# Optimization experiments

Measured on AMD Instinct MI355X. Metric: run time of the kernel, lower is better.

Reference implementation:

```python
import jax, jax.numpy as jnp
import numpy as np

N_NODES = 100000
N_EDGES = 800000
IN_DIM, HID_DIM, OUT_DIM = 128, 256, 128


def setup_inputs() -> dict:
    key = jax.random.key(0)
    k1, k2, k3, k4, k5 = jax.random.split(key, 5)
    x = jax.random.normal(k1, (N_NODES, IN_DIM), dtype=jnp.float32)
    edge_index = jax.random.randint(k2, (2, N_EDGES), 0, N_NODES, dtype=jnp.int64)
    edge_weight = jax.random.uniform(k3, (N_EDGES,), dtype=jnp.float32)
    W1 = jax.random.normal(k4, (IN_DIM, HID_DIM), dtype=jnp.float32) * 0.02
    b1 = jnp.zeros((HID_DIM,), dtype=jnp.float32)
    W2 = jax.random.normal(k5, (HID_DIM, OUT_DIM), dtype=jnp.float32) * 0.02
    b2 = jnp.zeros((OUT_DIM,), dtype=jnp.float32)
    return {"x": x, "edge_index": edge_index, "edge_weight": edge_weight,
            "W1": W1, "b1": b1, "W2": W2, "b2": b2}


def reference(x, edge_index, edge_weight, W1, b1, W2, b2):
    # GCNConv (normalize=True, add_self_loops=False), two layers with ReLU.
    # Dropout is identity at inference.
    row = edge_index[0]  # source nodes (E,)
    col = edge_index[1]  # target nodes (E,)
    n = x.shape[0]

    # Symmetric normalization: deg at target, norm = d^-1/2[row]*w*d^-1/2[col]
    deg = jax.ops.segment_sum(edge_weight, col, num_segments=n)  # (N,)
    dis = jnp.where(deg > 0, jax.lax.rsqrt(deg), 0.0)
    norm = dis[row] * edge_weight * dis[col]  # (E,)

    def gcn_conv(h, W, b):
        h = h @ W                                   # (N, F_out)
        msg = h[row] * norm[:, None]                # (E, F_out) gather+scale
        agg = jax.ops.segment_sum(msg, col, num_segments=n)  # scatter-add
        return agg + b

    h = jax.nn.relu(gcn_conv(x.astype(jnp.float32), W1, b1))
    return gcn_conv(h, W2, b2)
```

## Files before the change

### kernel.cpp

```cpp
#include <hip/hip_runtime.h>
#include <hip/hip_bf16.h>
#include <cstdint>
#include <cstddef>

#define N_NODES 100000
#define N_EDGES 800000
#define IN_DIM 128
#define HID_DIM 256
#define OUT_DIM 128

#define DEG_SCALE 2097152.0f
#define DEG_INV   (1.0f / 2097152.0f)

typedef __attribute__((ext_vector_type(8))) short bf16x8;
typedef __attribute__((ext_vector_type(4))) float f32x4;

__device__ __forceinline__ unsigned short f32_to_bf16(float f) {
    __hip_bfloat16 b = __float2bfloat16(f);
    return *reinterpret_cast<unsigned short*>(&b);
}
__device__ __forceinline__ float bf16_lo(uint32_t u) {
    uint32_t v = u << 16; return *reinterpret_cast<float*>(&v);
}
__device__ __forceinline__ float bf16_hi(uint32_t u) {
    uint32_t v = u & 0xffff0000u; return *reinterpret_cast<float*>(&v);
}

#define HIST_BLOCKS 3125
#define XB_BLOCKS 12500

__global__ void hist_prep_kernel(const int* __restrict__ ei,
                                 const float* __restrict__ ew,
                                 unsigned long long* __restrict__ cnt64,
                                 int* __restrict__ rank,
                                 const float* __restrict__ x,
                                 uint32_t* __restrict__ xb,
                                 const float* __restrict__ W1,
                                 unsigned short* __restrict__ W1F,
                                 const float* __restrict__ W2,
                                 unsigned short* __restrict__ W2F) {
    int b = blockIdx.x;
    if (b < HIST_BLOCKS) {
        int e = b * 256 + threadIdx.x;
        int c = ei[N_EDGES + e];
        uint32_t wfix = (uint32_t)(ew[e] * DEG_SCALE + 0.5f);
        unsigned long long add = (1ULL << 32) | (unsigned long long)wfix;
        unsigned long long old = atomicAdd(&cnt64[c], add);
        rank[e] = (int)(old >> 32);
        return;
    }
    b -= HIST_BLOCKS;
    if (b < XB_BLOCKS) {
        int i = b * 256 + threadIdx.x;
        float4 v = ((const float4*)x)[i];
        uint32_t lo = (uint32_t)f32_to_bf16(v.x) | ((uint32_t)f32_to_bf16(v.y) << 16);
        uint32_t hi = (uint32_t)f32_to_bf16(v.z) | ((uint32_t)f32_to_bf16(v.w) << 16);
        ((uint2*)xb)[i] = make_uint2(lo, hi);
    } else if (b < XB_BLOCKS + 128) {
        int idx = (b - XB_BLOCKS) * 256 + threadIdx.x;
        int j = idx & 7, lane = (idx >> 3) & 63;
        int nt = (idx >> 9) & 3, ks = (idx >> 11) & 3;
        int wc = (idx >> 13) & 1, nh = (idx >> 14) & 1;
        int fr = lane & 15, fq = lane >> 4;
        int row = nh * 128 + wc * 64 + nt * 16 + fr;
        int kk = ks * 32 + fq * 8 + j;
        W1F[idx] = f32_to_bf16(W1[kk * HID_DIM + row]);
    } else {
        int idx = (b - XB_BLOCKS - 128) * 256 + threadIdx.x;
        int j = idx & 7, lane = (idx >> 3) & 63;
        int nt = (idx >> 9) & 3, ks = (idx >> 11) & 3;
        int wc = (idx >> 13) & 1, nh = (idx >> 14) & 1;
        int fr = lane & 15, fq = lane >> 4;
        int n = wc * 64 + nt * 16 + fr;
        int kk = nh * 128 + ks * 32 + fq * 8 + j;
        W2F[idx] = f32_to_bf16(W2[kk * OUT_DIM + n]);
    }
}

__global__ void scan1_kernel(const unsigned long long* __restrict__ cnt64,
                             int* __restrict__ out, int* __restrict__ bsums,
                             float* __restrict__ dis, int n) {
    __shared__ int tmp[256];
    int t = threadIdx.x;
    int i = blockIdx.x * 256 + t;
    unsigned long long cv = (i < n) ? cnt64[i] : 0ULL;
    int v = (int)(cv >> 32);
    tmp[t] = v;
    __syncthreads();
    for (int off = 1; off < 256; off <<= 1) {
        int u = (t >= off) ? tmp[t - off] : 0;
        __syncthreads();
        tmp[t] += u;
        __syncthreads();
    }
    if (i < n) {
        out[i] = tmp[t] - v;
        uint32_t wf = (uint32_t)cv;
        dis[i] = wf ? rsqrtf((float)wf * DEG_INV) : 0.f;
    }
    if (t == 255) bsums[blockIdx.x] = tmp[255];
}

__global__ void scan23_kernel(int* __restrict__ rowp, const int* __restrict__ bsums,
                              int n, int total) {
    __shared__ int red[256];
    int b = blockIdx.x, t = threadIdx.x;
    int s = 0;
    for (int i = t; i < b; i += 256) s += bsums[i];
    red[t] = s;
    __syncthreads();
    for (int off = 128; off > 0; off >>= 1) {
        if (t < off) red[t] += red[t + off];
        __syncthreads();
    }
    int pre = red[0];
    int i = b * 256 + t;
    if (i == 0) rowp[n] = total;
    if (i < n) rowp[i] += pre;
}

__global__ void place_kernel(const int* __restrict__ ei,
                             const float* __restrict__ ew,
                             const int* __restrict__ rank,
                             const int* __restrict__ rowp,
                             const float* __restrict__ dis,
                             int2* __restrict__ pairs) {
    int e = blockIdx.x * 256 + threadIdx.x;
    if (e >= N_EDGES) return;
    int s = ei[e];
    int c = ei[N_EDGES + e];
    int pos = rowp[c] + rank[e];
    float wn = ew[e] * dis[s] * dis[c];
    pairs[pos] = make_int2(s, __float_as_int(wn));
}

__device__ __forceinline__ void acc_edge(float w, uint4 u, float* a) {
    a[0] += w * bf16_lo(u.x); a[1] += w * bf16_hi(u.x);
    a[2] += w * bf16_lo(u.y); a[3] += w * bf16_hi(u.y);
    a[4] += w * bf16_lo(u.z); a[5] += w * bf16_hi(u.z);
    a[6] += w * bf16_lo(u.w); a[7] += w * bf16_hi(u.w);
}

template <bool OUT_BF16>
__global__ void aggregate_kernel(const uint4* __restrict__ feat,
                                 const int* __restrict__ rowp,
                                 const int2* __restrict__ pairs,
                                 void* __restrict__ out_v,
                                 const float* __restrict__ bias) {
    int gtid = blockIdx.x * blockDim.x + threadIdx.x;
    int node = gtid >> 4;
    int lane = threadIdx.x & 15;
    if (node >= N_NODES) return;
    int beg = rowp[node], end = rowp[node + 1];
    float a[8] = {};

    int j = beg;
    for (; j + 8 <= end; j += 8) {
        int2 p[8]; uint4 u[8];
        #pragma unroll
        for (int q = 0; q < 8; ++q) p[q] = pairs[j + q];
        #pragma unroll
        for (int q = 0; q < 8; ++q) u[q] = feat[(size_t)p[q].x * 16 + lane];
        #pragma unroll
        for (int q = 0; q < 8; ++q) acc_edge(__int_as_float(p[q].y), u[q], a);
    }
    int r = end - j;
    if (r > 4) {
        int2 p[8]; uint4 u[8];
        #pragma unroll
        for (int q = 0; q < 8; ++q) {
            int idx = (j + q < end) ? j + q : beg;
            p[q] = pairs[idx];
        }
        #pragma unroll
        for (int q = 0; q < 8; ++q) u[q] = feat[(size_t)p[q].x * 16 + lane];
        #pragma unroll
        for (int q = 0; q < 8; ++q) {
            float w = (j + q < end) ? __int_as_float(p[q].y) : 0.f;
            acc_edge(w, u[q], a);
        }
    } else if (r > 0) {
        int2 p[4]; uint4 u[4];
        #pragma unroll
        for (int q = 0; q < 4; ++q) {
            int idx = (j + q < end) ? j + q : beg;
            p[q] = pairs[idx];
        }
        #pragma unroll
        for (int q = 0; q < 4; ++q) u[q] = feat[(size_t)p[q].x * 16 + lane];
        #pragma unroll
        for (int q = 0; q < 4; ++q) {
            float w = (j + q < end) ? __int_as_float(p[q].y) : 0.f;
            acc_edge(w, u[q], a);
        }
    }

    if (bias) {
        float4 b0 = ((const float4*)bias)[lane * 2];
        float4 b1 = ((const float4*)bias)[lane * 2 + 1];
        a[0] += b0.x; a[1] += b0.y; a[2] += b0.z; a[3] += b0.w;
        a[4] += b1.x; a[5] += b1.y; a[6] += b1.z; a[7] += b1.w;
    }
    if (OUT_BF16) {
        uint4 o;
        o.x = (uint32_t)f32_to_bf16(a[0]) | ((uint32_t)f32_to_bf16(a[1]) << 16);
        o.y = (uint32_t)f32_to_bf16(a[2]) | ((uint32_t)f32_to_bf16(a[3]) << 16);
        o.z = (uint32_t)f32_to_bf16(a[4]) | ((uint32_t)f32_to_bf16(a[5]) << 16);
        o.w = (uint32_t)f32_to_bf16(a[6]) | ((uint32_t)f32_to_bf16(a[7]) << 16);
        ((uint4*)out_v)[(size_t)node * 16 + lane] = o;
    } else {
        ((float4*)out_v)[(size_t)node * 32 + lane * 2] =
            make_float4(a[0], a[1], a[2], a[3]);
        ((float4*)out_v)[(size_t)node * 32 + lane * 2 + 1] =
            make_float4(a[4], a[5], a[6], a[7]);
    }
}

__global__ __launch_bounds__(256, 2) void gemm_fused_kernel(
    const unsigned short* __restrict__ A,
    const unsigned short* __restrict__ W1F,
    const float* __restrict__ b1,
    const unsigned short* __restrict__ W2F,
    unsigned short* __restrict__ T,
    int M) {
    __shared__ unsigned short As[128 * 128];
    __shared__ unsigned short Hs[128 * 136];
    int tid = threadIdx.x;
    int wave = tid >> 6, lane = tid & 63;
    int m0 = blockIdx.x * 128;
    int wr = (wave & 1) * 64;
    int wcid = wave >> 1;
    int wc = wcid * 64;
    int fr = lane & 15, fq = lane >> 4;

    #pragma unroll
    for (int i = 0; i < 8; ++i) {
        int cbase = (i * 4 + wave) * 64;
        int c = cbase + lane;
        int m = c >> 4, cl = c & 15;
        int qg = ((cl & 7) ^ (m & 7)) | (cl & 8);
        int gm = m0 + m; if (gm >= M) gm = M - 1;
        const unsigned short* ga = A + (size_t)gm * 128 + qg * 8;
        __builtin_amdgcn_global_load_lds(
            (const __attribute__((address_space(1))) void*)ga,
            (__attribute__((address_space(3))) void*)(As + (size_t)cbase * 8),
            16, 0, 0);
    }
    __syncthreads();

    bf16x8 af[4][4];
    #pragma unroll
    for (int ks = 0; ks < 4; ++ks) {
        int q = ks * 4 + fq;
        int cl = ((q & 7) ^ (fr & 7)) | (q & 8);
        #pragma unroll
        for (int mt = 0; mt < 4; ++mt)
            af[ks][mt] = *(const bf16x8*)(As + (wr + mt * 16 + fr) * 128 + cl * 8);
    }

    const bf16x8* w1p = (const bf16x8*)W1F;
    const bf16x8* w2p = (const bf16x8*)W2F;

    f32x4 acc_t[4][4] = {};
    #pragma unroll
    for (int nh = 0; nh < 2; ++nh) {
        int wbase = (nh * 2 + wcid) * 16 * 64;
        f32x4 acc_h[4][4] = {};
        #pragma unroll
        for (int ks = 0; ks < 4; ++ks) {
            bf16x8 wf[4];
            #pragma unroll
            for (int nt = 0; nt < 4; ++nt)
                wf[nt] = w1p[wbase + (ks * 4 + nt) * 64 + lane];
            #pragma unroll
            for (int mt = 0; mt < 4; ++mt)
                #pragma unroll
                for (int nt = 0; nt < 4; ++nt)
                    acc_h[mt][nt] = __builtin_amdgcn_mfma_f32_16x16x32_bf16(
                        af[ks][mt], wf[nt], acc_h[mt][nt], 0, 0, 0);
        }
        float bv[4];
        #pragma unroll
        for (int nt = 0; nt < 4; ++nt) bv[nt] = b1[nh * 128 + wc + nt * 16 + fr];
        __syncthreads();
        #pragma unroll
        for (int mt = 0; mt < 4; ++mt)
            #pragma unroll
            for (int r = 0; r < 4; ++r) {
                int row = wr + mt * 16 + fq * 4 + r;
                #pragma unroll
                for (int nt = 0; nt < 4; ++nt) {
                    float v = fmaxf(acc_h[mt][nt][r] + bv[nt], 0.f);
                    Hs[row * 136 + wc + nt * 16 + fr] = f32_to_bf16(v);
                }
            }
        __syncthreads();
        #pragma unroll
        for (int ks = 0; ks < 4; ++ks) {
            bf16x8 wf[4], hf[4];
            #pragma unroll
            for (int nt = 0; nt < 4; ++nt)
                wf[nt] = w2p[wbase + (ks * 4 + nt) * 64 + lane];
            #pragma unroll
            for (int mt = 0; mt < 4; ++mt)
                hf[mt] = *(const bf16x8*)(Hs + (wr + mt * 16 + fr) * 136 + ks * 32 + fq * 8);
            #pragma unroll
            for (int mt = 0; mt < 4; ++mt)
                #pragma unroll
                for (int nt = 0; nt < 4; ++nt)
                    acc_t[mt][nt] = __builtin_amdgcn_mfma_f32_16x16x32_bf16(
                        hf[mt], wf[nt], acc_t[mt][nt], 0, 0, 0);
        }
    }

    #pragma unroll
    for (int mt = 0; mt < 4; ++mt)
        #pragma unroll
        for (int r = 0; r < 4; ++r) {
            int row = m0 + wr + mt * 16 + fq * 4 + r;
            if (row >= M) continue;
            #pragma unroll
            for (int nt = 0; nt < 4; ++nt)
                T[(size_t)row * 128 + wc + nt * 16 + fr] = f32_to_bf16(acc_t[mt][nt][r]);
        }
}

extern "C" void kernel_launch(void* const* d_in, const int* in_sizes, int n_in,
                              void* d_out, int out_size, void* d_ws, size_t ws_size,
                              hipStream_t stream) {
    const float* x  = (const float*)d_in[0];
    const int*   ei = (const int*)d_in[1];
    const float* ew = (const float*)d_in[2];
    const float* W1 = (const float*)d_in[3];
    const float* b1 = (const float*)d_in[4];
    const float* W2 = (const float*)d_in[5];
    const float* b2 = (const float*)d_in[6];
    float* out = (float*)d_out;

    char* ws = (char*)d_ws;
    size_t off = 0;
    auto alloc = [&](size_t bytes) -> void* {
        void* p = ws + off;
        off = (off + bytes + 255) & ~(size_t)255;
        return p;
    };
    unsigned long long* cnt64 = (unsigned long long*)alloc((size_t)N_NODES * 8);
    float* dis   = (float*)alloc((size_t)N_NODES * 4);
    int*   rowp  = (int*)  alloc((size_t)(N_NODES + 1) * 4);
    int*   bsums = (int*)  alloc(512 * 4);
    int*   rank  = (int*)  alloc((size_t)N_EDGES * 4);
    int2*  pairs = (int2*) alloc((size_t)N_EDGES * 8);
    uint32_t* xb = (uint32_t*)alloc((size_t)N_NODES * IN_DIM * 2);
    unsigned short* W1F = (unsigned short*)alloc((size_t)IN_DIM * HID_DIM * 2);
    unsigned short* W2F = (unsigned short*)alloc((size_t)HID_DIM * OUT_DIM * 2);
    unsigned short* A1  = (unsigned short*)alloc((size_t)N_NODES * IN_DIM * 2);
    unsigned short* t   = (unsigned short*)alloc((size_t)N_NODES * OUT_DIM * 2);

    hipMemsetAsync(cnt64, 0, (size_t)N_NODES * 8, stream);

    int nn_blocks = (N_NODES + 255) / 256;
    int ne_blocks = (N_EDGES + 255) / 256;

    hist_prep_kernel<<<HIST_BLOCKS + XB_BLOCKS + 256, 256, 0, stream>>>(
        ei, ew, cnt64, rank, x, xb, W1, W1F, W2, W2F);

    scan1_kernel<<<nn_blocks, 256, 0, stream>>>(cnt64, rowp, bsums, dis, N_NODES);
    scan23_kernel<<<nn_blocks, 256, 0, stream>>>(rowp, bsums, N_NODES, N_EDGES);
    place_kernel<<<ne_blocks, 256, 0, stream>>>(ei, ew, rank, rowp, dis, pairs);

    int agg_blocks = (N_NODES * 16) / 256;

    aggregate_kernel<true><<<agg_blocks, 256, 0, stream>>>(
        (const uint4*)xb, rowp, pairs, A1, nullptr);

    gemm_fused_kernel<<<(N_NODES + 127) / 128, 256, 0, stream>>>(
        A1, W1F, b1, W2F, t, N_NODES);

    aggregate_kernel<false><<<agg_blocks, 256, 0, stream>>>(
        (const uint4*)t, rowp, pairs, out, b2);
}
```

Baseline: 274.6 us.

## Fuse preprocessing, scan, placement and first aggregation into a persistent grid-synced kernel

Replaces five separate launches (histogram/prep, two scan passes, edge placement, first aggregation) with one persistent kernel of 512 blocks that uses atomic-counter grid barriers between phases. It also folds the barrier-counter reset into the existing memset. The aim is to remove the launch gaps and tail effects between the short preprocessing kernels. In exchange, each phase runs on a fixed 512-block grid with grid-stride loops, and the spin barriers rely on all blocks being co-resident.

```diff
diff --git a/kernel.cpp b/kernel.cpp
--- a/kernel.cpp
+++ b/kernel.cpp
@@ -12,6 +12,9 @@
 #define DEG_SCALE 2097152.0f
 #define DEG_INV   (1.0f / 2097152.0f)
 
+#define MEGA_BLOCKS 512
+#define MEGA_GT (MEGA_BLOCKS * 256)
+
 typedef __attribute__((ext_vector_type(8))) short bf16x8;
 typedef __attribute__((ext_vector_type(4))) float f32x4;
 
@@ -26,112 +29,17 @@
     uint32_t v = u & 0xffff0000u; return *reinterpret_cast<float*>(&v);
 }
 
-#define HIST_BLOCKS 3125
-#define XB_BLOCKS 12500
-
-__global__ void hist_prep_kernel(const int* __restrict__ ei,
-                                 const float* __restrict__ ew,
-                                 unsigned long long* __restrict__ cnt64,
-                                 int* __restrict__ rank,
-                                 const float* __restrict__ x,
-                                 uint32_t* __restrict__ xb,
-                                 const float* __restrict__ W1,
-                                 unsigned short* __restrict__ W1F,
-                                 const float* __restrict__ W2,
-                                 unsigned short* __restrict__ W2F) {
-    int b = blockIdx.x;
-    if (b < HIST_BLOCKS) {
-        int e = b * 256 + threadIdx.x;
-        int c = ei[N_EDGES + e];
-        uint32_t wfix = (uint32_t)(ew[e] * DEG_SCALE + 0.5f);
-        unsigned long long add = (1ULL << 32) | (unsigned long long)wfix;
-        unsigned long long old = atomicAdd(&cnt64[c], add);
-        rank[e] = (int)(old >> 32);
-        return;
-    }
-    b -= HIST_BLOCKS;
-    if (b < XB_BLOCKS) {
-        int i = b * 256 + threadIdx.x;
-        float4 v = ((const float4*)x)[i];
-        uint32_t lo = (uint32_t)f32_to_bf16(v.x) | ((uint32_t)f32_to_bf16(v.y) << 16);
-        uint32_t hi = (uint32_t)f32_to_bf16(v.z) | ((uint32_t)f32_to_bf16(v.w) << 16);
-        ((uint2*)xb)[i] = make_uint2(lo, hi);
-    } else if (b < XB_BLOCKS + 128) {
-        int idx = (b - XB_BLOCKS) * 256 + threadIdx.x;
-        int j = idx & 7, lane = (idx >> 3) & 63;
-        int nt = (idx >> 9) & 3, ks = (idx >> 11) & 3;
-        int wc = (idx >> 13) & 1, nh = (idx >> 14) & 1;
-        int fr = lane & 15, fq = lane >> 4;
-        int row = nh * 128 + wc * 64 + nt * 16 + fr;
-        int kk = ks * 32 + fq * 8 + j;
-        W1F[idx] = f32_to_bf16(W1[kk * HID_DIM + row]);
-    } else {
-        int idx = (b - XB_BLOCKS - 128) * 256 + threadIdx.x;
-        int j = idx & 7, lane = (idx >> 3) & 63;
-        int nt = (idx >> 9) & 3, ks = (idx >> 11) & 3;
-        int wc = (idx >> 13) & 1, nh = (idx >> 14) & 1;
-        int fr = lane & 15, fq = lane >> 4;
-        int n = wc * 64 + nt * 16 + fr;
-        int kk = nh * 128 + ks * 32 + fq * 8 + j;
-        W2F[idx] = f32_to_bf16(W2[kk * OUT_DIM + n]);
-    }
-}
-
-__global__ void scan1_kernel(const unsigned long long* __restrict__ cnt64,
-                             int* __restrict__ out, int* __restrict__ bsums,
-                             float* __restrict__ dis, int n) {
-    __shared__ int tmp[256];
-    int t = threadIdx.x;
-    int i = blockIdx.x * 256 + t;
-    unsigned long long cv = (i < n) ? cnt64[i] : 0ULL;
-    int v = (int)(cv >> 32);
-    tmp[t] = v;
+__device__ __forceinline__ void grid_bar(unsigned int* b, unsigned int n) {
     __syncthreads();
-    for (int off = 1; off < 256; off <<= 1) {
-        int u = (t >= off) ? tmp[t - off] : 0;
-        __syncthreads();
-        tmp[t] += u;
-        __syncthreads();
-    }
-    if (i < n) {
-        out[i] = tmp[t] - v;
-        uint32_t wf = (uint32_t)cv;
-        dis[i] = wf ? rsqrtf((float)wf * DEG_INV) : 0.f;
-    }
-    if (t == 255) bsums[blockIdx.x] = tmp[255];
-}
-
-__global__ void scan23_kernel(int* __restrict__ rowp, const int* __restrict__ bsums,
-                              int n, int total) {
-    __shared__ int red[256];
-    int b = blockIdx.x, t = threadIdx.x;
-    int s = 0;
-    for (int i = t; i < b; i += 256) s += bsums[i];
-    red[t] = s;
+    if (threadIdx.x == 0) {
+        __threadfence();
+        atomicAdd(b, 1u);
+        while (__hip_atomic_load(b, __ATOMIC_RELAXED,
+                                 __HIP_MEMORY_SCOPE_AGENT) < n)
+            __builtin_amdgcn_s_sleep(2);
+        __threadfence();
+    }
     __syncthreads();
-    for (int off = 128; off > 0; off >>= 1) {
-        if (t < off) red[t] += red[t + off];
-        __syncthreads();
-    }
-    int pre = red[0];
-    int i = b * 256 + t;
-    if (i == 0) rowp[n] = total;
-    if (i < n) rowp[i] += pre;
-}
-
-__global__ void place_kernel(const int* __restrict__ ei,
-                             const float* __restrict__ ew,
-                             const int* __restrict__ rank,
-                             const int* __restrict__ rowp,
-                             const float* __restrict__ dis,
-                             int2* __restrict__ pairs) {
-    int e = blockIdx.x * 256 + threadIdx.x;
-    if (e >= N_EDGES) return;
-    int s = ei[e];
-    int c = ei[N_EDGES + e];
-    int pos = rowp[c] + rank[e];
-    float wn = ew[e] * dis[s] * dis[c];
-    pairs[pos] = make_int2(s, __float_as_int(wn));
 }
 
 __device__ __forceinline__ void acc_edge(float w, uint4 u, float* a) {
@@ -142,15 +50,12 @@
 }
 
 template <bool OUT_BF16>
-__global__ void aggregate_kernel(const uint4* __restrict__ feat,
-                                 const int* __restrict__ rowp,
-                                 const int2* __restrict__ pairs,
-                                 void* __restrict__ out_v,
-                                 const float* __restrict__ bias) {
-    int gtid = blockIdx.x * blockDim.x + threadIdx.x;
-    int node = gtid >> 4;
-    int lane = threadIdx.x & 15;
-    if (node >= N_NODES) return;
+__device__ __forceinline__ void agg_node(const uint4* __restrict__ feat,
+                                         const int* __restrict__ rowp,
+                                         const int2* __restrict__ pairs,
+                                         void* __restrict__ out_v,
+                                         const float* __restrict__ bias,
+                                         int node, int lane) {
     int beg = rowp[node], end = rowp[node + 1];
     float a[8] = {};
 
@@ -168,10 +73,7 @@
     if (r > 4) {
         int2 p[8]; uint4 u[8];
         #pragma unroll
-        for (int q = 0; q < 8; ++q) {
-            int idx = (j + q < end) ? j + q : beg;
-            p[q] = pairs[idx];
-        }
+        for (int q = 0; q < 8; ++q) p[q] = pairs[(j + q < end) ? j + q : end - 1];
         #pragma unroll
         for (int q = 0; q < 8; ++q) u[q] = feat[(size_t)p[q].x * 16 + lane];
         #pragma unroll
@@ -182,10 +84,7 @@
     } else if (r > 0) {
         int2 p[4]; uint4 u[4];
         #pragma unroll
-        for (int q = 0; q < 4; ++q) {
-            int idx = (j + q < end) ? j + q : beg;
-            p[q] = pairs[idx];
-        }
+        for (int q = 0; q < 4; ++q) p[q] = pairs[(j + q < end) ? j + q : end - 1];
         #pragma unroll
         for (int q = 0; q < 4; ++q) u[q] = feat[(size_t)p[q].x * 16 + lane];
         #pragma unroll
@@ -214,6 +113,114 @@
         ((float4*)out_v)[(size_t)node * 32 + lane * 2 + 1] =
             make_float4(a[4], a[5], a[6], a[7]);
     }
+}
+
+__global__ __launch_bounds__(256, 4) void mega_kernel(
+    const int* __restrict__ ei, const float* __restrict__ ew,
+    unsigned long long* __restrict__ cnt64, int* __restrict__ rank,
+    const float* __restrict__ x, uint32_t* __restrict__ xb,
+    const float* __restrict__ W1, unsigned short* __restrict__ W1F,
+    const float* __restrict__ W2, unsigned short* __restrict__ W2F,
+    int* __restrict__ rowp, int* __restrict__ bsums, float* __restrict__ dis,
+    int2* __restrict__ pairs, unsigned short* __restrict__ A1,
+    unsigned int* __restrict__ bar) {
+    __shared__ int tmp[256];
+    const int bid = blockIdx.x, tid = threadIdx.x;
+    const int gid0 = bid * 256 + tid;
+
+    for (int e = gid0; e < N_EDGES; e += MEGA_GT) {
+        int c = ei[N_EDGES + e];
+        uint32_t wfix = (uint32_t)(ew[e] * DEG_SCALE + 0.5f);
+        unsigned long long old =
+            atomicAdd(&cnt64[c], (1ULL << 32) | (unsigned long long)wfix);
+        rank[e] = (int)(old >> 32);
+    }
+    for (int i = gid0; i < N_NODES * IN_DIM / 4; i += MEGA_GT) {
+        float4 v = ((const float4*)x)[i];
+        uint32_t lo = (uint32_t)f32_to_bf16(v.x) | ((uint32_t)f32_to_bf16(v.y) << 16);
+        uint32_t hi = (uint32_t)f32_to_bf16(v.z) | ((uint32_t)f32_to_bf16(v.w) << 16);
+        ((uint2*)xb)[i] = make_uint2(lo, hi);
+    }
+    if (gid0 < 65536) {
+        int idx = gid0 & 32767;
+        int j = idx & 7, lane = (idx >> 3) & 63;
+        int nt = (idx >> 9) & 3, ks = (idx >> 11) & 3;
+        int wc = (idx >> 13) & 1, nh = (idx >> 14) & 1;
+        int fr = lane & 15, fq = lane >> 4;
+        if (gid0 < 32768) {
+            int row = nh * 128 + wc * 64 + nt * 16 + fr;
+            int kk = ks * 32 + fq * 8 + j;
+            W1F[idx] = f32_to_bf16(W1[kk * HID_DIM + row]);
+        } else {
+            int n = wc * 64 + nt * 16 + fr;
+            int kk = nh * 128 + ks * 32 + fq * 8 + j;
+            W2F[idx] = f32_to_bf16(W2[kk * OUT_DIM + n]);
+        }
+    }
+    grid_bar(&bar[0], MEGA_BLOCKS);
+
+    if (bid < 391) {
+        int i = bid * 256 + tid;
+        unsigned long long cv = (i < N_NODES) ? cnt64[i] : 0ULL;
+        int v = (int)(cv >> 32);
+        tmp[tid] = v;
+        __syncthreads();
+        for (int off = 1; off < 256; off <<= 1) {
+            int u = (tid >= off) ? tmp[tid - off] : 0;
+            __syncthreads();
+            tmp[tid] += u;
+            __syncthreads();
+        }
+        if (i < N_NODES) {
+            rowp[i] = tmp[tid] - v;
+            uint32_t wf = (uint32_t)cv;
+            dis[i] = wf ? rsqrtf((float)wf * DEG_INV) : 0.f;
+        }
+        if (tid == 255) bsums[bid] = tmp[255];
+    }
+    grid_bar(&bar[1], MEGA_BLOCKS);
+
+    if (bid < 391) {
+        int s = 0;
+        for (int i = tid; i < bid; i += 256) s += bsums[i];
+        tmp[tid] = s;
+        __syncthreads();
+        for (int off = 128; off > 0; off >>= 1) {
+            if (tid < off) tmp[tid] += tmp[tid + off];
+            __syncthreads();
+        }
+        int pre = tmp[0];
+        int i = bid * 256 + tid;
+        if (i == 0) rowp[N_NODES] = N_EDGES;
+        if (i < N_NODES) rowp[i] += pre;
+    }
+    grid_bar(&bar[2], MEGA_BLOCKS);
+
+    for (int e = gid0; e < N_EDGES; e += MEGA_GT) {
+        int s = ei[e];
+        int c = ei[N_EDGES + e];
+        int pos = rowp[c] + rank[e];
+        float wn = ew[e] * dis[s] * dis[c];
+        pairs[pos] = make_int2(s, __float_as_int(wn));
+    }
+    grid_bar(&bar[3], MEGA_BLOCKS);
+
+    for (int g = gid0; g < N_NODES * 16; g += MEGA_GT) {
+        agg_node<true>((const uint4*)xb, rowp, pairs, A1, nullptr,
+                       g >> 4, g & 15);
+    }
+}
+
+template <bool OUT_BF16>
+__global__ void aggregate_kernel(const uint4* __restrict__ feat,
+                                 const int* __restrict__ rowp,
+                                 const int2* __restrict__ pairs,
+                                 void* __restrict__ out_v,
+                                 const float* __restrict__ bias) {
+    int gtid = blockIdx.x * blockDim.x + threadIdx.x;
+    int node = gtid >> 4;
+    if (node >= N_NODES) return;
+    agg_node<OUT_BF16>(feat, rowp, pairs, out_v, bias, node, threadIdx.x & 15);
 }
 
 __global__ __launch_bounds__(256, 2) void gemm_fused_kernel(
@@ -344,6 +351,7 @@
         off = (off + bytes + 255) & ~(size_t)255;
         return p;
     };
+    unsigned int* bar = (unsigned int*)alloc(256);
     unsigned long long* cnt64 = (unsigned long long*)alloc((size_t)N_NODES * 8);
     float* dis   = (float*)alloc((size_t)N_NODES * 4);
     int*   rowp  = (int*)  alloc((size_t)(N_NODES + 1) * 4);
@@ -356,26 +364,16 @@
     unsigned short* A1  = (unsigned short*)alloc((size_t)N_NODES * IN_DIM * 2);
     unsigned short* t   = (unsigned short*)alloc((size_t)N_NODES * OUT_DIM * 2);
 
-    hipMemsetAsync(cnt64, 0, (size_t)N_NODES * 8, stream);
-
-    int nn_blocks = (N_NODES + 255) / 256;
-    int ne_blocks = (N_EDGES + 255) / 256;
-
-    hist_prep_kernel<<<HIST_BLOCKS + XB_BLOCKS + 256, 256, 0, stream>>>(
-        ei, ew, cnt64, rank, x, xb, W1, W1F, W2, W2F);
-
-    scan1_kernel<<<nn_blocks, 256, 0, stream>>>(cnt64, rowp, bsums, dis, N_NODES);
-    scan23_kernel<<<nn_blocks, 256, 0, stream>>>(rowp, bsums, N_NODES, N_EDGES);
-    place_kernel<<<ne_blocks, 256, 0, stream>>>(ei, ew, rank, rowp, dis, pairs);
-
-    int agg_blocks = (N_NODES * 16) / 256;
-
-    aggregate_kernel<true><<<agg_blocks, 256, 0, stream>>>(
-        (const uint4*)xb, rowp, pairs, A1, nullptr);
+    hipMemsetAsync(bar, 0, 256 + (size_t)N_NODES * 8, stream);
+
+    mega_kernel<<<MEGA_BLOCKS, 256, 0, stream>>>(
+        ei, ew, cnt64, rank, x, xb, W1, W1F, W2, W2F,
+        rowp, bsums, dis, pairs, A1, bar);
 
     gemm_fused_kernel<<<(N_NODES + 127) / 128, 256, 0, stream>>>(
         A1, W1F, b1, W2F, t, N_NODES);
 
+    int agg_blocks = (N_NODES * 16) / 256;
     aggregate_kernel<false><<<agg_blocks, 256, 0, stream>>>(
         (const uint4*)t, rowp, pairs, out, b2);
 }
```

Measured after the change: 493.0 us. +79.6%, slower.

## Fuse first-layer aggregation into GEMM kernel, building A tile in LDS

Applied to the files above, without the earlier changes.

The first sparse aggregation (gather of bf16 x rows weighted by norm) now runs inside the fused GEMM kernel. Each block aggregates its 128 nodes directly into the swizzled LDS A tile, removing the A1 intermediate buffer, its global write and reload, and one kernel launch. The cost is lower parallelism and latency hiding for the gather: only 782 blocks at 2 per CU, with 4-wide inner batches instead of 8. Tail padding indices now repeat end-1 instead of beg.

```diff
diff --git a/kernel.cpp b/kernel.cpp
--- a/kernel.cpp
+++ b/kernel.cpp
@@ -168,10 +168,7 @@
     if (r > 4) {
         int2 p[8]; uint4 u[8];
         #pragma unroll
-        for (int q = 0; q < 8; ++q) {
-            int idx = (j + q < end) ? j + q : beg;
-            p[q] = pairs[idx];
-        }
+        for (int q = 0; q < 8; ++q) p[q] = pairs[(j + q < end) ? j + q : end - 1];
         #pragma unroll
         for (int q = 0; q < 8; ++q) u[q] = feat[(size_t)p[q].x * 16 + lane];
         #pragma unroll
@@ -182,10 +179,7 @@
     } else if (r > 0) {
         int2 p[4]; uint4 u[4];
         #pragma unroll
-        for (int q = 0; q < 4; ++q) {
-            int idx = (j + q < end) ? j + q : beg;
-            p[q] = pairs[idx];
-        }
+        for (int q = 0; q < 4; ++q) p[q] = pairs[(j + q < end) ? j + q : end - 1];
         #pragma unroll
         for (int q = 0; q < 4; ++q) u[q] = feat[(size_t)p[q].x * 16 + lane];
         #pragma unroll
@@ -216,14 +210,16 @@
     }
 }
 
-__global__ __launch_bounds__(256, 2) void gemm_fused_kernel(
-    const unsigned short* __restrict__ A,
+__global__ __launch_bounds__(256, 2) void gemm_agg_fused_kernel(
+    const uint32_t* __restrict__ xb,
+    const int* __restrict__ rowp,
+    const int2* __restrict__ pairs,
     const unsigned short* __restrict__ W1F,
     const float* __restrict__ b1,
     const unsigned short* __restrict__ W2F,
     unsigned short* __restrict__ T,
     int M) {
-    __shared__ unsigned short As[128 * 128];
+    __shared__ __align__(16) unsigned short As[128 * 128];
     __shared__ unsigned short Hs[128 * 136];
     int tid = threadIdx.x;
     int wave = tid >> 6, lane = tid & 63;
@@ -233,18 +229,36 @@
     int wc = wcid * 64;
     int fr = lane & 15, fq = lane >> 4;
 
-    #pragma unroll
-    for (int i = 0; i < 8; ++i) {
-        int cbase = (i * 4 + wave) * 64;
-        int c = cbase + lane;
-        int m = c >> 4, cl = c & 15;
-        int qg = ((cl & 7) ^ (m & 7)) | (cl & 8);
-        int gm = m0 + m; if (gm >= M) gm = M - 1;
-        const unsigned short* ga = A + (size_t)gm * 128 + qg * 8;
-        __builtin_amdgcn_global_load_lds(
-            (const __attribute__((address_space(1))) void*)ga,
-            (__attribute__((address_space(3))) void*)(As + (size_t)cbase * 8),
-            16, 0, 0);
+    {
+        int glane = tid & 15;
+        #pragma unroll
+        for (int rnd = 0; rnd < 8; ++rnd) {
+            int m = rnd * 16 + (tid >> 4);
+            int node = m0 + m; if (node >= M) node = M - 1;
+            int beg = rowp[node], end = rowp[node + 1];
+            float a[8] = {};
+            for (int j = beg; j < end; j += 4) {
+                int2 p[4]; uint4 u[4];
+                #pragma unroll
+                for (int q = 0; q < 4; ++q)
+                    p[q] = pairs[(j + q < end) ? j + q : end - 1];
+                #pragma unroll
+                for (int q = 0; q < 4; ++q)
+                    u[q] = ((const uint4*)xb)[(size_t)p[q].x * 16 + glane];
+                #pragma unroll
+                for (int q = 0; q < 4; ++q) {
+                    float w = (j + q < end) ? __int_as_float(p[q].y) : 0.f;
+                    acc_edge(w, u[q], a);
+                }
+            }
+            uint4 o;
+            o.x = (uint32_t)f32_to_bf16(a[0]) | ((uint32_t)f32_to_bf16(a[1]) << 16);
+            o.y = (uint32_t)f32_to_bf16(a[2]) | ((uint32_t)f32_to_bf16(a[3]) << 16);
+            o.z = (uint32_t)f32_to_bf16(a[4]) | ((uint32_t)f32_to_bf16(a[5]) << 16);
+            o.w = (uint32_t)f32_to_bf16(a[6]) | ((uint32_t)f32_to_bf16(a[7]) << 16);
+            int cl = ((glane & 7) ^ (m & 7)) | (glane & 8);
+            *reinterpret_cast<uint4*>(&As[(m * 16 + cl) * 8]) = o;
+        }
     }
     __syncthreads();
 
@@ -353,7 +367,6 @@
     uint32_t* xb = (uint32_t*)alloc((size_t)N_NODES * IN_DIM * 2);
     unsigned short* W1F = (unsigned short*)alloc((size_t)IN_DIM * HID_DIM * 2);
     unsigned short* W2F = (unsigned short*)alloc((size_t)HID_DIM * OUT_DIM * 2);
-    unsigned short* A1  = (unsigned short*)alloc((size_t)N_NODES * IN_DIM * 2);
     unsigned short* t   = (unsigned short*)alloc((size_t)N_NODES * OUT_DIM * 2);
 
     hipMemsetAsync(cnt64, 0, (size_t)N_NODES * 8, stream);
@@ -368,14 +381,10 @@
     scan23_kernel<<<nn_blocks, 256, 0, stream>>>(rowp, bsums, N_NODES, N_EDGES);
     place_kernel<<<ne_blocks, 256, 0, stream>>>(ei, ew, rank, rowp, dis, pairs);
 
+    gemm_agg_fused_kernel<<<(N_NODES + 127) / 128, 256, 0, stream>>>(
+        xb, rowp, pairs, W1F, b1, W2F, t, N_NODES);
+
     int agg_blocks = (N_NODES * 16) / 256;
-
-    aggregate_kernel<true><<<agg_blocks, 256, 0, stream>>>(
-        (const uint4*)xb, rowp, pairs, A1, nullptr);
-
-    gemm_fused_kernel<<<(N_NODES + 127) / 128, 256, 0, stream>>>(
-        A1, W1F, b1, W2F, t, N_NODES);
-
     aggregate_kernel<false><<<agg_blocks, 256, 0, stream>>>(
         (const uint4*)t, rowp, pairs, out, b2);
 }
```

Measured after the change: 282.2 us. 1.03x slower.

## Replace two-pass scan with single-pass decoupled look-back prefix scan

Applied to the files above, without the earlier changes.

Merges the block-local scan and the separate block-offset fix-up kernel into one kernel that uses decoupled look-back: each block publishes its aggregate and inclusive prefix in a status array, and a single wavefront polls its predecessors. This saves a kernel launch and a second pass over the row pointer array. The status array is cleared by extending the existing memset, which is valid because it sits directly after cnt64 at a 256-byte-aligned offset. The look-back relies on earlier blocks being scheduled first, since it spin-waits on their flags. Tail padding in the aggregation now reads the last valid edge instead of the first one.

```diff
diff --git a/kernel.cpp b/kernel.cpp
--- a/kernel.cpp
+++ b/kernel.cpp
@@ -77,12 +77,13 @@
     }
 }
 
-__global__ void scan1_kernel(const unsigned long long* __restrict__ cnt64,
-                             int* __restrict__ out, int* __restrict__ bsums,
-                             float* __restrict__ dis, int n) {
+__global__ void scan_kernel(const unsigned long long* __restrict__ cnt64,
+                            int* __restrict__ rowp, float* __restrict__ dis,
+                            unsigned long long* __restrict__ status, int n) {
     __shared__ int tmp[256];
-    int t = threadIdx.x;
-    int i = blockIdx.x * 256 + t;
+    __shared__ unsigned int sprefix;
+    const int bid = blockIdx.x, t = threadIdx.x;
+    int i = bid * 256 + t;
     unsigned long long cv = (i < n) ? cnt64[i] : 0ULL;
     int v = (int)(cv >> 32);
     tmp[t] = v;
@@ -93,30 +94,58 @@
         tmp[t] += u;
         __syncthreads();
     }
+    unsigned int total = (unsigned int)tmp[255];
+
+    if (t == 0)
+        __hip_atomic_store(&status[bid],
+                           ((unsigned long long)total << 2) | 1ULL,
+                           __ATOMIC_RELEASE, __HIP_MEMORY_SCOPE_AGENT);
+
+    if (t < 64) {
+        unsigned int sum = 0;
+        int base = bid - 1;
+        while (base >= 0) {
+            int idx = base - t;
+            unsigned long long s = 0;
+            if (idx >= 0) {
+                do {
+                    s = __hip_atomic_load(&status[idx], __ATOMIC_ACQUIRE,
+                                          __HIP_MEMORY_SCOPE_AGENT);
+                } while ((s & 3ULL) == 0ULL);
+            }
+            unsigned long long pm = __ballot(idx >= 0 && (s & 3ULL) == 2ULL);
+            unsigned int c;
+            if (pm) {
+                int fp = __ffsll(pm) - 1;
+                c = (idx >= 0 && t <= fp) ? (unsigned int)(s >> 2) : 0u;
+                #pragma unroll
+                for (int o = 32; o > 0; o >>= 1) c += __shfl_down(c, o);
+                if (t == 0) sum += c;
+                break;
+            } else {
+                c = (idx >= 0) ? (unsigned int)(s >> 2) : 0u;
+                #pragma unroll
+                for (int o = 32; o > 0; o >>= 1) c += __shfl_down(c, o);
+                if (t == 0) sum += c;
+                base -= 64;
+            }
+        }
+        if (t == 0) {
+            sprefix = sum;
+            __hip_atomic_store(&status[bid],
+                               ((unsigned long long)(sum + total) << 2) | 2ULL,
+                               __ATOMIC_RELEASE, __HIP_MEMORY_SCOPE_AGENT);
+        }
+    }
+    __syncthreads();
+    unsigned int pre = sprefix;
+
     if (i < n) {
-        out[i] = tmp[t] - v;
+        rowp[i] = (int)(pre + (unsigned int)tmp[t] - (unsigned int)v);
         uint32_t wf = (uint32_t)cv;
         dis[i] = wf ? rsqrtf((float)wf * DEG_INV) : 0.f;
     }
-    if (t == 255) bsums[blockIdx.x] = tmp[255];
-}
-
-__global__ void scan23_kernel(int* __restrict__ rowp, const int* __restrict__ bsums,
-                              int n, int total) {
-    __shared__ int red[256];
-    int b = blockIdx.x, t = threadIdx.x;
-    int s = 0;
-    for (int i = t; i < b; i += 256) s += bsums[i];
-    red[t] = s;
-    __syncthreads();
-    for (int off = 128; off > 0; off >>= 1) {
-        if (t < off) red[t] += red[t + off];
-        __syncthreads();
-    }
-    int pre = red[0];
-    int i = b * 256 + t;
-    if (i == 0) rowp[n] = total;
-    if (i < n) rowp[i] += pre;
+    if (i == 0) rowp[n] = N_EDGES;
 }
 
 __global__ void place_kernel(const int* __restrict__ ei,
@@ -168,10 +197,7 @@
     if (r > 4) {
         int2 p[8]; uint4 u[8];
         #pragma unroll
-        for (int q = 0; q < 8; ++q) {
-            int idx = (j + q < end) ? j + q : beg;
-            p[q] = pairs[idx];
-        }
+        for (int q = 0; q < 8; ++q) p[q] = pairs[(j + q < end) ? j + q : end - 1];
         #pragma unroll
         for (int q = 0; q < 8; ++q) u[q] = feat[(size_t)p[q].x * 16 + lane];
         #pragma unroll
@@ -182,10 +208,7 @@
     } else if (r > 0) {
         int2 p[4]; uint4 u[4];
         #pragma unroll
-        for (int q = 0; q < 4; ++q) {
-            int idx = (j + q < end) ? j + q : beg;
-            p[q] = pairs[idx];
-        }
+        for (int q = 0; q < 4; ++q) p[q] = pairs[(j + q < end) ? j + q : end - 1];
         #pragma unroll
         for (int q = 0; q < 4; ++q) u[q] = feat[(size_t)p[q].x * 16 + lane];
         #pragma unroll
@@ -344,10 +367,10 @@
         off = (off + bytes + 255) & ~(size_t)255;
         return p;
     };
-    unsigned long long* cnt64 = (unsigned long long*)alloc((size_t)N_NODES * 8);
+    unsigned long long* cnt64  = (unsigned long long*)alloc((size_t)N_NODES * 8);
+    unsigned long long* status = (unsigned long long*)alloc(512 * 8);
     float* dis   = (float*)alloc((size_t)N_NODES * 4);
     int*   rowp  = (int*)  alloc((size_t)(N_NODES + 1) * 4);
-    int*   bsums = (int*)  alloc(512 * 4);
     int*   rank  = (int*)  alloc((size_t)N_EDGES * 4);
     int2*  pairs = (int2*) alloc((size_t)N_EDGES * 8);
     uint32_t* xb = (uint32_t*)alloc((size_t)N_NODES * IN_DIM * 2);
@@ -356,7 +379,7 @@
     unsigned short* A1  = (unsigned short*)alloc((size_t)N_NODES * IN_DIM * 2);
     unsigned short* t   = (unsigned short*)alloc((size_t)N_NODES * OUT_DIM * 2);
 
-    hipMemsetAsync(cnt64, 0, (size_t)N_NODES * 8, stream);
+    hipMemsetAsync(cnt64, 0, (size_t)N_NODES * 8 + 512 * 8, stream);
 
     int nn_blocks = (N_NODES + 255) / 256;
     int ne_blocks = (N_EDGES + 255) / 256;
@@ -364,8 +387,8 @@
     hist_prep_kernel<<<HIST_BLOCKS + XB_BLOCKS + 256, 256, 0, stream>>>(
         ei, ew, cnt64, rank, x, xb, W1, W1F, W2, W2F);
 
-    scan1_kernel<<<nn_blocks, 256, 0, stream>>>(cnt64, rowp, bsums, dis, N_NODES);
-    scan23_kernel<<<nn_blocks, 256, 0, stream>>>(rowp, bsums, N_NODES, N_EDGES);
+    scan_kernel<<<nn_blocks, 256, 0, stream>>>(cnt64, rowp, dis, status, N_NODES);
+
     place_kernel<<<ne_blocks, 256, 0, stream>>>(ei, ew, rank, rowp, dis, pairs);
 
     int agg_blocks = (N_NODES * 16) / 256;
```

Measured after the change: 283.3 us. 3.2% more time.
